# Optimization experiments

Hardware: AMD Instinct MI355X
Metric: run time of the kernel (lower is better)

Reference implementation:

```python
import jax, jax.numpy as jnp
import numpy as np

B, S, D = 4, 1024, 1024
H, HD = 16, 64  # num_heads, head_dim; H*HD == D (qkv_features)
NEG_BIG = -1e10


def setup_inputs() -> dict:
    key = jax.random.key(0)
    ks = jax.random.split(key, 16)
    inp = {
        'inputs_q': jax.random.normal(ks[0], (B, S, D), jnp.float32),
        'inputs_kv': jax.random.normal(ks[1], (B, S, D), jnp.float32),
        'pos_emb_q': jax.random.normal(ks[2], (B, S, D), jnp.float32),
        'pos_emb_k': jax.random.normal(ks[3], (B, S, D), jnp.float32),
        'pos_emb_v': jax.random.normal(ks[4], (B, S, D), jnp.float32),
        'key_padding_mask': jnp.ones((B, S), jnp.float32),
    }
    scale = 1.0 / np.sqrt(D)
    inp['wq'] = jax.random.normal(ks[5], (D, H, HD), jnp.float32) * scale
    inp['bq'] = jnp.zeros((H, HD), jnp.float32)
    inp['wk'] = jax.random.normal(ks[6], (D, H, HD), jnp.float32) * scale
    inp['bk'] = jnp.zeros((H, HD), jnp.float32)
    inp['wv'] = jax.random.normal(ks[7], (D, H, HD), jnp.float32) * scale
    inp['bv'] = jnp.zeros((H, HD), jnp.float32)
    inp['wo'] = jax.random.normal(ks[8], (H, HD, D), jnp.float32) * scale
    inp['bo'] = jnp.zeros((D,), jnp.float32)
    return inp


def reference(inputs_q, inputs_kv, pos_emb_q, pos_emb_k, pos_emb_v,
              key_padding_mask, wq, bq, wk, bk, wv, bv, wo, bo):
    # Add positional embeddings before QKV projections (DETR style).
    q_in = inputs_q + pos_emb_q
    k_in = inputs_kv + pos_emb_k
    v_in = inputs_kv + pos_emb_v
    # DenseGeneral: [b,s,f] x [f,h,d] -> [b,s,h,d]
    q = jnp.einsum('bsf,fhd->bshd', q_in, wq) + bq
    k = jnp.einsum('bsf,fhd->bshd', k_in, wk) + bk
    v = jnp.einsum('bsf,fhd->bshd', v_in, wv) + bv
    # Additive key-padding bias, broadcast to [b,1,1,kv].
    bias = ((1.0 - key_padding_mask) * NEG_BIG)[:, None, None, :]
    q = q / jnp.sqrt(jnp.asarray(HD, q.dtype))
    attn = jnp.einsum('bqhd,bkhd->bhqk', q, k) + bias
    attn = jax.nn.softmax(attn, axis=-1)
    # (train=False: no dropout; identity capture layer is a no-op.)
    x = jnp.einsum('bhqk,bkhd->bqhd', attn, v)
    # Output projection over (heads, head_dim).
    out = jnp.einsum('bqhd,hdf->bqf', x, wo) + bo
    return out
```

## Files before the change

kernel.cpp:

```cpp
#include <hip/hip_runtime.h>
#include <hip/hip_bf16.h>
#include <stdint.h>

typedef __bf16 bf16_t;
typedef __bf16 bf16x8 __attribute__((ext_vector_type(8)));
typedef __bf16 bf16x4v __attribute__((ext_vector_type(4)));
typedef float  f32x4  __attribute__((ext_vector_type(4)));
typedef float  f32x16 __attribute__((ext_vector_type(16)));
typedef unsigned int u32;
typedef u32 u32x4 __attribute__((ext_vector_type(4)));

#define NEG_BIG (-1e10f)

__device__ __forceinline__ void load_lds16(const void* gsrc, void* ldst) {
  __builtin_amdgcn_global_load_lds(
      (__attribute__((address_space(1))) void*)(gsrc),
      (__attribute__((address_space(3))) void*)(ldst), 16, 0, 0);
}

__device__ __forceinline__ u32 cvt_pk_bf16(float lo, float hi) {
  u32 r;
  asm("v_cvt_pk_bf16_f32 %0, %1, %2" : "=v"(r) : "v"(lo), "v"(hi));
  return r;
}

__global__ __launch_bounds__(256) void k_prep(
    const float4* __restrict__ iq, const float4* __restrict__ ikv,
    const float4* __restrict__ pq, const float4* __restrict__ pk,
    const float4* __restrict__ pv,
    bf16_t* __restrict__ Xq, bf16_t* __restrict__ Xk, bf16_t* __restrict__ Xv)
{
  int i = blockIdx.x * 256 + threadIdx.x;
  float4 a = iq[i], b = ikv[i];
  float4 eq = pq[i], ek = pk[i], ev = pv[i];
  bf16x4v q, k, v;
  q[0] = (bf16_t)(a.x + eq.x); q[1] = (bf16_t)(a.y + eq.y);
  q[2] = (bf16_t)(a.z + eq.z); q[3] = (bf16_t)(a.w + eq.w);
  k[0] = (bf16_t)(b.x + ek.x); k[1] = (bf16_t)(b.y + ek.y);
  k[2] = (bf16_t)(b.z + ek.z); k[3] = (bf16_t)(b.w + ek.w);
  v[0] = (bf16_t)(b.x + ev.x); v[1] = (bf16_t)(b.y + ev.y);
  v[2] = (bf16_t)(b.z + ev.z); v[3] = (bf16_t)(b.w + ev.w);
  *(bf16x4v*)&Xq[(size_t)i*4] = q;
  *(bf16x4v*)&Xk[(size_t)i*4] = k;
  *(bf16x4v*)&Xv[(size_t)i*4] = v;
}

__global__ __launch_bounds__(256) void k_wtrans(
    const float* __restrict__ wq, const float* __restrict__ wk,
    const float* __restrict__ wv, const float* __restrict__ wo,
    bf16_t* __restrict__ Wqt, bf16_t* __restrict__ Wkt,
    bf16_t* __restrict__ Wvt, bf16_t* __restrict__ Wot)
{
  __shared__ float t[64][65];
  int z = blockIdx.z;
  const float* src = z==0 ? wq : z==1 ? wk : z==2 ? wv : wo;
  bf16_t*      dst = z==0 ? Wqt : z==1 ? Wkt : z==2 ? Wvt : Wot;
  int n0 = blockIdx.x * 64, k0 = blockIdx.y * 64;
  int c = threadIdx.x & 63, rb = threadIdx.x >> 6;
  #pragma unroll
  for (int i = 0; i < 16; ++i) {
    int r = i*4 + rb;
    t[r][c] = src[(size_t)(k0 + r)*1024 + n0 + c];
  }
  __syncthreads();
  #pragma unroll
  for (int i = 0; i < 16; ++i) {
    int r = i*4 + rb;
    dst[(size_t)(n0 + r)*1024 + k0 + c] = (bf16_t)t[c][r];
  }
}

__global__ __launch_bounds__(256, 2) void k_gemm_qkv(
    const bf16_t* __restrict__ Xq, const bf16_t* __restrict__ Xk, const bf16_t* __restrict__ Xv,
    const bf16_t* __restrict__ Wqt, const bf16_t* __restrict__ Wkt, const bf16_t* __restrict__ Wvt,
    const float* __restrict__ bq, const float* __restrict__ bk, const float* __restrict__ bv,
    bf16_t* __restrict__ Qo, bf16_t* __restrict__ Ko, bf16_t* __restrict__ Vo)
{
  int z = blockIdx.z;
  const bf16_t* A  = z==0 ? Xq : z==1 ? Xk : Xv;
  const bf16_t* Bt = z==0 ? Wqt : z==1 ? Wkt : Wvt;
  const float* bias = z==0 ? bq : z==1 ? bk : bv;
  bf16_t* C = z==0 ? Qo : z==1 ? Ko : Vo;
  const float scale = (z==0) ? 0.125f : 1.0f;

  __shared__ bf16_t As[128*64];
  __shared__ bf16_t Bs[128*64];

  const int tid = threadIdx.x, lane = tid & 63, wid = tid >> 6;
  const int wm = wid >> 1, wn = wid & 1;
  const int bm0 = blockIdx.y * 128, bn0 = blockIdx.x * 128;
  const int g = lane >> 4, c = lane & 15;

  f32x4 acc[4][4] = {};

  const int srow = wid*32 + (lane >> 3);
  const int sch  = lane & 7;

  for (int kt = 0; kt < 16; ++kt) {
    int k0 = kt * 64;
    #pragma unroll
    for (int i = 0; i < 4; ++i) {
      int r  = srow + i*8;
      int ca = sch ^ (r & 7);
      load_lds16(A  + (size_t)(bm0 + r)*1024 + k0 + ca*8, &As[(wid*32 + i*8)*64]);
      load_lds16(Bt + (size_t)(bn0 + r)*1024 + k0 + ca*8, &Bs[(wid*32 + i*8)*64]);
    }
    __syncthreads();
    #pragma unroll
    for (int kk = 0; kk < 2; ++kk) {
      bf16x8 af[4], bfr[4];
      #pragma unroll
      for (int m = 0; m < 4; ++m) {
        int row = wm*64 + m*16 + c;
        int ch  = (kk*4 + g) ^ (row & 7);
        af[m] = *(const bf16x8*)&As[row*64 + ch*8];
      }
      #pragma unroll
      for (int n = 0; n < 4; ++n) {
        int row = wn*64 + n*16 + c;
        int ch  = (kk*4 + g) ^ (row & 7);
        bfr[n] = *(const bf16x8*)&Bs[row*64 + ch*8];
      }
      #pragma unroll
      for (int m = 0; m < 4; ++m)
        #pragma unroll
        for (int n = 0; n < 4; ++n)
          acc[m][n] = __builtin_amdgcn_mfma_f32_16x16x32_bf16(af[m], bfr[n], acc[m][n], 0, 0, 0);
    }
    __syncthreads();
  }

  #pragma unroll
  for (int n = 0; n < 4; ++n) {
    int col = bn0 + wn*64 + n*16 + c;
    float bn_ = bias[col];
    #pragma unroll
    for (int m = 0; m < 4; ++m) {
      int row0 = bm0 + wm*64 + m*16 + g*4;
      #pragma unroll
      for (int r = 0; r < 4; ++r) {
        float v = (acc[m][n][r] + bn_) * scale;
        C[(size_t)(row0 + r)*1024 + col] = (bf16_t)v;
      }
    }
  }
}

__global__ __launch_bounds__(256) void k_vtrans(
    const bf16_t* __restrict__ V, bf16_t* __restrict__ Vt)
{
  __shared__ uint32_t t[64][65];
  int bh = blockIdx.y;
  int s0 = blockIdx.x * 64;
  int b = bh >> 4, h = bh & 15;
  int c = threadIdx.x & 63, rb = threadIdx.x >> 6;
  const uint16_t* src = (const uint16_t*)V + (size_t)(b*1024 + s0)*1024 + h*64;
  #pragma unroll
  for (int i = 0; i < 16; ++i) {
    int r = i*4 + rb;
    t[r][c] = src[(size_t)r*1024 + c];
  }
  __syncthreads();
  uint16_t* dst = (uint16_t*)Vt + (size_t)(bh*64)*1024 + s0;
  #pragma unroll
  for (int i = 0; i < 16; ++i) {
    int r = i*4 + rb;
    dst[(size_t)r*1024 + c] = (uint16_t)t[c][r];
  }
}

__global__ __launch_bounds__(256, 2) void k_attn2(
    const bf16_t* __restrict__ Qm, const bf16_t* __restrict__ Km,
    const bf16_t* __restrict__ Vt, const float* __restrict__ mask,
    bf16_t* __restrict__ X2)
{
  __shared__ bf16_t Ks[2][64*64];
  __shared__ bf16_t Vs[2][64*64];
  __shared__ float  bias_lds[1024];
  __shared__ float  l_lds[4][32];

  const int qt = blockIdx.x, h = blockIdx.y, b = blockIdx.z;
  const int tid = threadIdx.x, lane = tid & 63, wid = tid >> 6;
  const int lq = lane & 31;
  const int hi = lane >> 5;

  {
    float4 m4 = *(const float4*)&mask[b*1024 + tid*4];
    float4 b4;
    b4.x = (1.0f - m4.x) * NEG_BIG;
    b4.y = (1.0f - m4.y) * NEG_BIG;
    b4.z = (1.0f - m4.z) * NEG_BIG;
    b4.w = (1.0f - m4.w) * NEG_BIG;
    *(float4*)&bias_lds[tid*4] = b4;
  }

  const int q0w = qt*128 + wid*32;
  bf16x8 qf[4];
  #pragma unroll
  for (int kb = 0; kb < 4; ++kb)
    qf[kb] = *(const bf16x8*)&Qm[(size_t)(b*1024 + q0w + lq)*1024 + h*64 + kb*16 + hi*8];

  f32x16 oacc[2] = {};
  float mrow = -1e30f, lsum = 0.f;

  const int sr8 = (lane >> 3);
  const int sc8 = lane & 7;
  #define STAGE(bufi, kv0)                                                        \
    {                                                                             \
      _Pragma("unroll")                                                           \
      for (int cc = 0; cc < 2; ++cc) {                                            \
        int r  = cc*32 + wid*8 + sr8;                                             \
        int ca = sc8 ^ (r & 7);                                                   \
        load_lds16(Km + (size_t)(b*1024 + (kv0) + r)*1024 + h*64 + ca*8,          \
                   &Ks[bufi][(cc*32 + wid*8)*64]);                                \
        load_lds16(Vt + (size_t)((b*16 + h)*64 + r)*1024 + (kv0) + ca*8,          \
                   &Vs[bufi][(cc*32 + wid*8)*64]);                                \
      }                                                                           \
    }

  STAGE(0, 0);
  __syncthreads();

  for (int kt = 0; kt < 16; ++kt) {
    const int buf = kt & 1;
    if (kt < 15) STAGE(buf ^ 1, (kt + 1) * 64);

    f32x16 s[2];
    #pragma unroll
    for (int blk = 0; blk < 2; ++blk) {
      f32x16 acc = {};
      #pragma unroll
      for (int kb = 0; kb < 4; ++kb) {
        int row = blk*32 + lq;
        int ch  = (kb*2 + hi) ^ (row & 7);
        bf16x8 kf = *(const bf16x8*)&Ks[buf][row*64 + ch*8];
        acc = __builtin_amdgcn_mfma_f32_32x32x16_bf16(kf, qf[kb], acc, 0, 0, 0);
      }
      s[blk] = acc;
    }

    #pragma unroll
    for (int blk = 0; blk < 2; ++blk)
      #pragma unroll
      for (int g2 = 0; g2 < 4; ++g2) {
        float4 b4 = *(const float4*)&bias_lds[kt*64 + blk*32 + g2*8 + hi*4];
        s[blk][g2*4+0] += b4.x;
        s[blk][g2*4+1] += b4.y;
        s[blk][g2*4+2] += b4.z;
        s[blk][g2*4+3] += b4.w;
      }

    float pmax = s[0][0];
    #pragma unroll
    for (int blk = 0; blk < 2; ++blk)
      #pragma unroll
      for (int r = 0; r < 16; ++r) pmax = fmaxf(pmax, s[blk][r]);
    pmax = fmaxf(pmax, __shfl_xor(pmax, 32, 64));

    if (!__all(pmax - mrow <= 8.0f)) {
      float mnew = fmaxf(mrow, pmax);
      float sc = __expf(mrow - mnew);
      lsum *= sc;
      #pragma unroll
      for (int nb = 0; nb < 2; ++nb)
        #pragma unroll
        for (int i = 0; i < 16; ++i) oacc[nb][i] *= sc;
      mrow = mnew;
    }

    float rs = 0.f;
    #pragma unroll
    for (int blk = 0; blk < 2; ++blk)
      #pragma unroll
      for (int r = 0; r < 16; ++r) {
        float p = __expf(s[blk][r] - mrow);
        s[blk][r] = p;
        rs += p;
      }
    lsum += rs + __shfl_xor(rs, 32, 64);

    u32 paw[4][4];
    #pragma unroll
    for (int blk = 0; blk < 2; ++blk)
      #pragma unroll
      for (int half = 0; half < 2; ++half) {
        int base = half * 8;
        #pragma unroll
        for (int w = 0; w < 2; ++w) {
          u32 x = cvt_pk_bf16(s[blk][base + 2*w],     s[blk][base + 2*w + 1]);
          u32 y = cvt_pk_bf16(s[blk][base + 4 + 2*w], s[blk][base + 4 + 2*w + 1]);
          asm("v_permlane32_swap_b32 %0, %1" : "+v"(x), "+v"(y));
          paw[blk*2 + half][w]     = x;
          paw[blk*2 + half][w + 2] = y;
        }
      }

    #pragma unroll
    for (int ks = 0; ks < 4; ++ks) {
      u32x4 t = { paw[ks][0], paw[ks][1], paw[ks][2], paw[ks][3] };
      bf16x8 pa = __builtin_bit_cast(bf16x8, t);
      #pragma unroll
      for (int nb = 0; nb < 2; ++nb) {
        int row = nb*32 + lq;
        int ch  = (ks*2 + hi) ^ (row & 7);
        bf16x8 vf = *(const bf16x8*)&Vs[buf][row*64 + ch*8];
        oacc[nb] = __builtin_amdgcn_mfma_f32_32x32x16_bf16(pa, vf, oacc[nb], 0, 0, 0);
      }
    }
    __syncthreads();
  }

  l_lds[wid][lq] = lsum;
  __syncthreads();
  #pragma unroll
  for (int g2 = 0; g2 < 4; ++g2)
    #pragma unroll
    for (int j = 0; j < 4; ++j) {
      int reg  = g2*4 + j;
      int qrow = j + 8*g2 + 4*hi;
      float inv = 1.0f / l_lds[wid][qrow];
      #pragma unroll
      for (int nb = 0; nb < 2; ++nb)
        X2[(size_t)(b*1024 + q0w + qrow)*1024 + h*64 + nb*32 + lq] =
            (bf16_t)(oacc[nb][reg] * inv);
    }
  #undef STAGE
}

__global__ __launch_bounds__(256, 2) void k_gemm_out(
    const bf16_t* __restrict__ A, const bf16_t* __restrict__ Bt,
    const float* __restrict__ bo, float* __restrict__ C)
{
  __shared__ bf16_t As[128*64];
  __shared__ bf16_t Bs[128*64];

  const int tid = threadIdx.x, lane = tid & 63, wid = tid >> 6;
  const int wm = wid >> 1, wn = wid & 1;
  const int bm0 = blockIdx.y * 128, bn0 = blockIdx.x * 128;
  const int g = lane >> 4, c = lane & 15;

  f32x4 acc[4][4] = {};
  const int srow = wid*32 + (lane >> 3);
  const int sch  = lane & 7;

  for (int kt = 0; kt < 16; ++kt) {
    int k0 = kt * 64;
    #pragma unroll
    for (int i = 0; i < 4; ++i) {
      int r  = srow + i*8;
      int ca = sch ^ (r & 7);
      load_lds16(A  + (size_t)(bm0 + r)*1024 + k0 + ca*8, &As[(wid*32 + i*8)*64]);
      load_lds16(Bt + (size_t)(bn0 + r)*1024 + k0 + ca*8, &Bs[(wid*32 + i*8)*64]);
    }
    __syncthreads();
    #pragma unroll
    for (int kk = 0; kk < 2; ++kk) {
      bf16x8 af[4], bfr[4];
      #pragma unroll
      for (int m = 0; m < 4; ++m) {
        int row = wm*64 + m*16 + c;
        int ch  = (kk*4 + g) ^ (row & 7);
        af[m] = *(const bf16x8*)&As[row*64 + ch*8];
      }
      #pragma unroll
      for (int n = 0; n < 4; ++n) {
        int row = wn*64 + n*16 + c;
        int ch  = (kk*4 + g) ^ (row & 7);
        bfr[n] = *(const bf16x8*)&Bs[row*64 + ch*8];
      }
      #pragma unroll
      for (int m = 0; m < 4; ++m)
        #pragma unroll
        for (int n = 0; n < 4; ++n)
          acc[m][n] = __builtin_amdgcn_mfma_f32_16x16x32_bf16(af[m], bfr[n], acc[m][n], 0, 0, 0);
    }
    __syncthreads();
  }

  #pragma unroll
  for (int n = 0; n < 4; ++n) {
    int col = bn0 + wn*64 + n*16 + c;
    float bn_ = bo[col];
    #pragma unroll
    for (int m = 0; m < 4; ++m) {
      int row0 = bm0 + wm*64 + m*16 + g*4;
      #pragma unroll
      for (int r = 0; r < 4; ++r)
        C[(size_t)(row0 + r)*1024 + col] = acc[m][n][r] + bn_;
    }
  }
}

extern "C" void kernel_launch(void* const* d_in, const int* in_sizes, int n_in,
                              void* d_out, int out_size, void* d_ws, size_t ws_size,
                              hipStream_t stream) {
  const float* iq   = (const float*)d_in[0];
  const float* ikv  = (const float*)d_in[1];
  const float* pq   = (const float*)d_in[2];
  const float* pk   = (const float*)d_in[3];
  const float* pv   = (const float*)d_in[4];
  const float* mask = (const float*)d_in[5];
  const float* wq   = (const float*)d_in[6];
  const float* bq   = (const float*)d_in[7];
  const float* wk   = (const float*)d_in[8];
  const float* bk   = (const float*)d_in[9];
  const float* wv   = (const float*)d_in[10];
  const float* bv   = (const float*)d_in[11];
  const float* wo   = (const float*)d_in[12];
  const float* bo   = (const float*)d_in[13];
  float* out = (float*)d_out;

  char* ws = (char*)d_ws;
  bf16_t* Xq  = (bf16_t*)(ws + (size_t)( 0u<<20));
  bf16_t* Xk  = (bf16_t*)(ws + (size_t)( 8u<<20));
  bf16_t* Xv  = (bf16_t*)(ws + (size_t)(16u<<20));
  bf16_t* Wqt = (bf16_t*)(ws + (size_t)(24u<<20));
  bf16_t* Wkt = (bf16_t*)(ws + (size_t)(26u<<20));
  bf16_t* Wvt = (bf16_t*)(ws + (size_t)(28u<<20));
  bf16_t* Wot = (bf16_t*)(ws + (size_t)(30u<<20));
  bf16_t* Q   = (bf16_t*)(ws + (size_t)(32u<<20));
  bf16_t* K   = (bf16_t*)(ws + (size_t)(40u<<20));
  bf16_t* V   = (bf16_t*)(ws + (size_t)(48u<<20));
  bf16_t* Vt  = (bf16_t*)(ws + (size_t)(56u<<20));
  bf16_t* X2  = (bf16_t*)(ws + (size_t)(64u<<20));

  k_prep<<<4096, 256, 0, stream>>>((const float4*)iq, (const float4*)ikv,
      (const float4*)pq, (const float4*)pk, (const float4*)pv, Xq, Xk, Xv);
  k_wtrans<<<dim3(16,16,4), 256, 0, stream>>>(wq, wk, wv, wo, Wqt, Wkt, Wvt, Wot);
  k_gemm_qkv<<<dim3(8,32,3), 256, 0, stream>>>(Xq, Xk, Xv, Wqt, Wkt, Wvt,
                                               bq, bk, bv, Q, K, V);
  k_vtrans<<<dim3(16,64), 256, 0, stream>>>(V, Vt);
  k_attn2<<<dim3(8,16,4), 256, 0, stream>>>(Q, K, Vt, mask, X2);
  k_gemm_out<<<dim3(8,32), 256, 0, stream>>>(X2, Wot, bo, out);
}
```

Baseline: 122.0 us.

## Fuse embedding add into QKV GEMM, double-buffer LDS, remap block order

```diff
diff --git a/kernel.cpp b/kernel.cpp
--- a/kernel.cpp
+++ b/kernel.cpp
@@ -4,7 +4,6 @@
 
 typedef __bf16 bf16_t;
 typedef __bf16 bf16x8 __attribute__((ext_vector_type(8)));
-typedef __bf16 bf16x4v __attribute__((ext_vector_type(4)));
 typedef float  f32x4  __attribute__((ext_vector_type(4)));
 typedef float  f32x16 __attribute__((ext_vector_type(16)));
 typedef unsigned int u32;
@@ -22,27 +21,6 @@
   u32 r;
   asm("v_cvt_pk_bf16_f32 %0, %1, %2" : "=v"(r) : "v"(lo), "v"(hi));
   return r;
-}
-
-__global__ __launch_bounds__(256) void k_prep(
-    const float4* __restrict__ iq, const float4* __restrict__ ikv,
-    const float4* __restrict__ pq, const float4* __restrict__ pk,
-    const float4* __restrict__ pv,
-    bf16_t* __restrict__ Xq, bf16_t* __restrict__ Xk, bf16_t* __restrict__ Xv)
-{
-  int i = blockIdx.x * 256 + threadIdx.x;
-  float4 a = iq[i], b = ikv[i];
-  float4 eq = pq[i], ek = pk[i], ev = pv[i];
-  bf16x4v q, k, v;
-  q[0] = (bf16_t)(a.x + eq.x); q[1] = (bf16_t)(a.y + eq.y);
-  q[2] = (bf16_t)(a.z + eq.z); q[3] = (bf16_t)(a.w + eq.w);
-  k[0] = (bf16_t)(b.x + ek.x); k[1] = (bf16_t)(b.y + ek.y);
-  k[2] = (bf16_t)(b.z + ek.z); k[3] = (bf16_t)(b.w + ek.w);
-  v[0] = (bf16_t)(b.x + ev.x); v[1] = (bf16_t)(b.y + ev.y);
-  v[2] = (bf16_t)(b.z + ev.z); v[3] = (bf16_t)(b.w + ev.w);
-  *(bf16x4v*)&Xq[(size_t)i*4] = q;
-  *(bf16x4v*)&Xk[(size_t)i*4] = k;
-  *(bf16x4v*)&Xv[(size_t)i*4] = v;
 }
 
 __global__ __launch_bounds__(256) void k_wtrans(
@@ -71,41 +49,79 @@
 }
 
 __global__ __launch_bounds__(256, 2) void k_gemm_qkv(
-    const bf16_t* __restrict__ Xq, const bf16_t* __restrict__ Xk, const bf16_t* __restrict__ Xv,
+    const float* __restrict__ iq, const float* __restrict__ ikv,
+    const float* __restrict__ pq, const float* __restrict__ pk, const float* __restrict__ pv,
     const bf16_t* __restrict__ Wqt, const bf16_t* __restrict__ Wkt, const bf16_t* __restrict__ Wvt,
     const float* __restrict__ bq, const float* __restrict__ bk, const float* __restrict__ bv,
     bf16_t* __restrict__ Qo, bf16_t* __restrict__ Ko, bf16_t* __restrict__ Vo)
 {
-  int z = blockIdx.z;
-  const bf16_t* A  = z==0 ? Xq : z==1 ? Xk : Xv;
-  const bf16_t* Bt = z==0 ? Wqt : z==1 ? Wkt : Wvt;
-  const float* bias = z==0 ? bq : z==1 ? bk : bv;
-  bf16_t* C = z==0 ? Qo : z==1 ? Ko : Vo;
-  const float scale = (z==0) ? 0.125f : 1.0f;
-
-  __shared__ bf16_t As[128*64];
-  __shared__ bf16_t Bs[128*64];
+  const int L = blockIdx.x + (blockIdx.y << 3) + (blockIdx.z << 8);
+  const int w = (L & 7) * 96 + (L >> 3);
+  const int bx = w & 7, by = (w >> 3) & 31, bz = w >> 8;
+
+  const float* Ain  = bz==0 ? iq : ikv;
+  const float* Pin  = bz==0 ? pq : (bz==1 ? pk : pv);
+  const bf16_t* Bt  = bz==0 ? Wqt : bz==1 ? Wkt : Wvt;
+  const float* bias = bz==0 ? bq : bz==1 ? bk : bv;
+  bf16_t* C = bz==0 ? Qo : bz==1 ? Ko : Vo;
+  const float scale = (bz==0) ? 0.125f : 1.0f;
+
+  __shared__ bf16_t As[2][128*64];
+  __shared__ bf16_t Bs[2][128*64];
 
   const int tid = threadIdx.x, lane = tid & 63, wid = tid >> 6;
   const int wm = wid >> 1, wn = wid & 1;
-  const int bm0 = blockIdx.y * 128, bn0 = blockIdx.x * 128;
+  const int bm0 = by * 128, bn0 = bx * 128;
   const int g = lane >> 4, c = lane & 15;
 
   f32x4 acc[4][4] = {};
 
-  const int srow = wid*32 + (lane >> 3);
-  const int sch  = lane & 7;
+  const int sr  = lane >> 3;
+  const int sch = lane & 7;
+
+  f32x4 ar[4][2], pr[4][2];
+
+  #define ISSUE_A(kt_)                                                           \
+    { _Pragma("unroll")                                                          \
+      for (int i = 0; i < 4; ++i) {                                              \
+        int r = wid*32 + i*8 + sr;                                               \
+        size_t off = (size_t)(bm0 + r)*1024 + (size_t)(kt_)*64 + sch*8;          \
+        ar[i][0] = *(const f32x4*)&Ain[off];                                     \
+        ar[i][1] = *(const f32x4*)&Ain[off + 4];                                 \
+        pr[i][0] = *(const f32x4*)&Pin[off];                                     \
+        pr[i][1] = *(const f32x4*)&Pin[off + 4];                                 \
+      } }
+
+  #define WRITE_A(bufi)                                                          \
+    { _Pragma("unroll")                                                          \
+      for (int i = 0; i < 4; ++i) {                                              \
+        int r = wid*32 + i*8 + sr;                                               \
+        bf16x8 v;                                                                \
+        _Pragma("unroll")                                                        \
+        for (int e = 0; e < 4; ++e) {                                            \
+          v[e]     = (bf16_t)(ar[i][0][e] + pr[i][0][e]);                        \
+          v[e + 4] = (bf16_t)(ar[i][1][e] + pr[i][1][e]);                        \
+        }                                                                        \
+        *(bf16x8*)&As[bufi][r*64 + ((sch ^ (r & 7)))*8] = v;                     \
+      } }
+
+  #define ISSUE_B(bufi, kt_)                                                     \
+    { _Pragma("unroll")                                                          \
+      for (int i = 0; i < 4; ++i) {                                              \
+        int r  = wid*32 + i*8 + sr;                                              \
+        int ca = sch ^ (r & 7);                                                  \
+        load_lds16(Bt + (size_t)(bn0 + r)*1024 + (size_t)(kt_)*64 + ca*8,        \
+                   &Bs[bufi][(wid*32 + i*8)*64]);                                \
+      } }
+
+  ISSUE_A(0); ISSUE_B(0, 0);
+  WRITE_A(0);
+  __syncthreads();
 
   for (int kt = 0; kt < 16; ++kt) {
-    int k0 = kt * 64;
-    #pragma unroll
-    for (int i = 0; i < 4; ++i) {
-      int r  = srow + i*8;
-      int ca = sch ^ (r & 7);
-      load_lds16(A  + (size_t)(bm0 + r)*1024 + k0 + ca*8, &As[(wid*32 + i*8)*64]);
-      load_lds16(Bt + (size_t)(bn0 + r)*1024 + k0 + ca*8, &Bs[(wid*32 + i*8)*64]);
-    }
-    __syncthreads();
+    const int buf = kt & 1;
+    if (kt < 15) { ISSUE_A(kt + 1); ISSUE_B(buf ^ 1, kt + 1); }
+
     #pragma unroll
     for (int kk = 0; kk < 2; ++kk) {
       bf16x8 af[4], bfr[4];
@@ -113,13 +129,13 @@
       for (int m = 0; m < 4; ++m) {
         int row = wm*64 + m*16 + c;
         int ch  = (kk*4 + g) ^ (row & 7);
-        af[m] = *(const bf16x8*)&As[row*64 + ch*8];
+        af[m] = *(const bf16x8*)&As[buf][row*64 + ch*8];
       }
       #pragma unroll
       for (int n = 0; n < 4; ++n) {
         int row = wn*64 + n*16 + c;
         int ch  = (kk*4 + g) ^ (row & 7);
-        bfr[n] = *(const bf16x8*)&Bs[row*64 + ch*8];
+        bfr[n] = *(const bf16x8*)&Bs[buf][row*64 + ch*8];
       }
       #pragma unroll
       for (int m = 0; m < 4; ++m)
@@ -127,7 +143,11 @@
         for (int n = 0; n < 4; ++n)
           acc[m][n] = __builtin_amdgcn_mfma_f32_16x16x32_bf16(af[m], bfr[n], acc[m][n], 0, 0, 0);
     }
-    __syncthreads();
+
+    if (kt < 15) {
+      WRITE_A(buf ^ 1);
+      __syncthreads();
+    }
   }
 
   #pragma unroll
@@ -144,6 +164,9 @@
       }
     }
   }
+  #undef ISSUE_A
+  #undef WRITE_A
+  #undef ISSUE_B
 }
 
 __global__ __launch_bounds__(256) void k_vtrans(
@@ -286,12 +309,12 @@
       for (int half = 0; half < 2; ++half) {
         int base = half * 8;
         #pragma unroll
-        for (int w = 0; w < 2; ++w) {
-          u32 x = cvt_pk_bf16(s[blk][base + 2*w],     s[blk][base + 2*w + 1]);
-          u32 y = cvt_pk_bf16(s[blk][base + 4 + 2*w], s[blk][base + 4 + 2*w + 1]);
+        for (int w2 = 0; w2 < 2; ++w2) {
+          u32 x = cvt_pk_bf16(s[blk][base + 2*w2],     s[blk][base + 2*w2 + 1]);
+          u32 y = cvt_pk_bf16(s[blk][base + 4 + 2*w2], s[blk][base + 4 + 2*w2 + 1]);
           asm("v_permlane32_swap_b32 %0, %1" : "+v"(x), "+v"(y));
-          paw[blk*2 + half][w]     = x;
-          paw[blk*2 + half][w + 2] = y;
+          paw[blk*2 + half][w2]     = x;
+          paw[blk*2 + half][w2 + 2] = y;
         }
       }
 
@@ -331,28 +354,40 @@
     const bf16_t* __restrict__ A, const bf16_t* __restrict__ Bt,
     const float* __restrict__ bo, float* __restrict__ C)
 {
-  __shared__ bf16_t As[128*64];
-  __shared__ bf16_t Bs[128*64];
+  const int L = blockIdx.x + (blockIdx.y << 3);
+  const int w = (L & 7) * 32 + (L >> 3);
+  const int bx = w & 7, by = w >> 3;
+
+  __shared__ bf16_t As[2][128*64];
+  __shared__ bf16_t Bs[2][128*64];
 
   const int tid = threadIdx.x, lane = tid & 63, wid = tid >> 6;
   const int wm = wid >> 1, wn = wid & 1;
-  const int bm0 = blockIdx.y * 128, bn0 = blockIdx.x * 128;
+  const int bm0 = by * 128, bn0 = bx * 128;
   const int g = lane >> 4, c = lane & 15;
 
   f32x4 acc[4][4] = {};
-  const int srow = wid*32 + (lane >> 3);
-  const int sch  = lane & 7;
+  const int sr  = lane >> 3;
+  const int sch = lane & 7;
+
+  #define STAGEO(bufi, kt_)                                                      \
+    { _Pragma("unroll")                                                          \
+      for (int i = 0; i < 4; ++i) {                                              \
+        int r  = wid*32 + i*8 + sr;                                              \
+        int ca = sch ^ (r & 7);                                                  \
+        load_lds16(A  + (size_t)(bm0 + r)*1024 + (size_t)(kt_)*64 + ca*8,        \
+                   &As[bufi][(wid*32 + i*8)*64]);                                \
+        load_lds16(Bt + (size_t)(bn0 + r)*1024 + (size_t)(kt_)*64 + ca*8,        \
+                   &Bs[bufi][(wid*32 + i*8)*64]);                                \
+      } }
+
+  STAGEO(0, 0);
+  __syncthreads();
 
   for (int kt = 0; kt < 16; ++kt) {
-    int k0 = kt * 64;
-    #pragma unroll
-    for (int i = 0; i < 4; ++i) {
-      int r  = srow + i*8;
-      int ca = sch ^ (r & 7);
-      load_lds16(A  + (size_t)(bm0 + r)*1024 + k0 + ca*8, &As[(wid*32 + i*8)*64]);
-      load_lds16(Bt + (size_t)(bn0 + r)*1024 + k0 + ca*8, &Bs[(wid*32 + i*8)*64]);
-    }
-    __syncthreads();
+    const int buf = kt & 1;
+    if (kt < 15) STAGEO(buf ^ 1, kt + 1);
+
     #pragma unroll
     for (int kk = 0; kk < 2; ++kk) {
       bf16x8 af[4], bfr[4];
@@ -360,13 +395,13 @@
       for (int m = 0; m < 4; ++m) {
         int row = wm*64 + m*16 + c;
         int ch  = (kk*4 + g) ^ (row & 7);
-        af[m] = *(const bf16x8*)&As[row*64 + ch*8];
+        af[m] = *(const bf16x8*)&As[buf][row*64 + ch*8];
       }
       #pragma unroll
       for (int n = 0; n < 4; ++n) {
         int row = wn*64 + n*16 + c;
         int ch  = (kk*4 + g) ^ (row & 7);
-        bfr[n] = *(const bf16x8*)&Bs[row*64 + ch*8];
+        bfr[n] = *(const bf16x8*)&Bs[buf][row*64 + ch*8];
       }
       #pragma unroll
       for (int m = 0; m < 4; ++m)
@@ -374,7 +409,7 @@
         for (int n = 0; n < 4; ++n)
           acc[m][n] = __builtin_amdgcn_mfma_f32_16x16x32_bf16(af[m], bfr[n], acc[m][n], 0, 0, 0);
     }
-    __syncthreads();
+    if (kt < 15) __syncthreads();
   }
 
   #pragma unroll
@@ -389,6 +424,7 @@
         C[(size_t)(row0 + r)*1024 + col] = acc[m][n][r] + bn_;
     }
   }
+  #undef STAGEO
 }
 
 extern "C" void kernel_launch(void* const* d_in, const int* in_sizes, int n_in,
@@ -411,9 +447,6 @@
   float* out = (float*)d_out;
 
   char* ws = (char*)d_ws;
-  bf16_t* Xq  = (bf16_t*)(ws + (size_t)( 0u<<20));
-  bf16_t* Xk  = (bf16_t*)(ws + (size_t)( 8u<<20));
-  bf16_t* Xv  = (bf16_t*)(ws + (size_t)(16u<<20));
   bf16_t* Wqt = (bf16_t*)(ws + (size_t)(24u<<20));
   bf16_t* Wkt = (bf16_t*)(ws + (size_t)(26u<<20));
   bf16_t* Wvt = (bf16_t*)(ws + (size_t)(28u<<20));
@@ -424,11 +457,9 @@
   bf16_t* Vt  = (bf16_t*)(ws + (size_t)(56u<<20));
   bf16_t* X2  = (bf16_t*)(ws + (size_t)(64u<<20));
 
-  k_prep<<<4096, 256, 0, stream>>>((const float4*)iq, (const float4*)ikv,
-      (const float4*)pq, (const float4*)pk, (const float4*)pv, Xq, Xk, Xv);
   k_wtrans<<<dim3(16,16,4), 256, 0, stream>>>(wq, wk, wv, wo, Wqt, Wkt, Wvt, Wot);
-  k_gemm_qkv<<<dim3(8,32,3), 256, 0, stream>>>(Xq, Xk, Xv, Wqt, Wkt, Wvt,
-                                               bq, bk, bv, Q, K, V);
+  k_gemm_qkv<<<dim3(8,32,3), 256, 0, stream>>>(iq, ikv, pq, pk, pv,
+                                               Wqt, Wkt, Wvt, bq, bk, bv, Q, K, V);
   k_vtrans<<<dim3(16,64), 256, 0, stream>>>(V, Vt);
   k_attn2<<<dim3(8,16,4), 256, 0, stream>>>(Q, K, Vt, mask, X2);
   k_gemm_out<<<dim3(8,32), 256, 0, stream>>>(X2, Wot, bo, out);
```

Result: slower. 147.9 us (+21.2%).
